# Kernel tuning notes

Hardware: AMD Instinct MI355X
Metric: run time of the kernel (lower is better)

## Reference

```python
import jax, jax.numpy as jnp
import numpy as np

D, HID, C = 300, 64, 21          # Dict_size, hidden_size, cell_size
B, H, W = 4, 144, 144

def gelu(x):
    return jax.nn.gelu(x, approximate=False)  # torch nn.GELU default (erf)

def c1x1(x, w, b):
    # 1x1 conv == pointwise matmul over channels: x [b,c,h,w], w [o,c], b [o]
    return jnp.einsum('bchw,oc->bohw', x, w) + b[None, :, None, None]

def gconv(x, w, b):
    return gelu(c1x1(x, w, b))


def setup_inputs() -> dict:
    key = jax.random.key(0)
    ks = iter(jax.random.split(key, 40))
    def Wm(o, i):
        return jax.random.normal(next(ks), (o, i), jnp.float32) * 0.05
    def bv(o):
        return jax.random.normal(next(ks), (o,), jnp.float32) * 0.01
    inp = {'y': jax.random.normal(next(ks), (B, C, H, W), jnp.float32)}
    # cell_size -> Dict_size encoders
    for nm in ['we1', 'we2', 'wfy1', 'wiy1', 'wfy2', 'wiy2']:
        inp[nm + '_w'] = Wm(D, C); inp[nm + '_b'] = bv(D)
    # Dict_size -> Dict_size recurrent convs
    for nm in ['wd1', 'wd2', 'wfx1', 'wix1', 'wfx2', 'wix2']:
        inp[nm + '_w'] = Wm(D, D); inp[nm + '_b'] = bv(D)
    # Line1 head: 3x3 valid conv D->2*HID, then 1x1 2*HID->2*HID, 1x1 2*HID->1
    inp['line_w1'] = jax.random.normal(next(ks), (2 * HID, D, 3, 3), jnp.float32) * 0.05
    inp['line_b1'] = bv(2 * HID)
    inp['line_w2'] = Wm(2 * HID, 2 * HID); inp['line_b2'] = bv(2 * HID)
    inp['line_w3'] = Wm(1, 2 * HID);       inp['line_b3'] = bv(1)
    return inp


def reference(y, we1_w, we1_b, we2_w, we2_b, wfy1_w, wfy1_b, wiy1_w, wiy1_b,
              wfy2_w, wfy2_b, wiy2_w, wiy2_b, wd1_w, wd1_b, wd2_w, wd2_b,
              wfx1_w, wfx1_b, wix1_w, wix1_b, wfx2_w, wfx2_b, wix2_w, wix2_b,
              line_w1, line_b1, line_w2, line_b2, line_w3, line_b3):
    ywe1 = gconv(y, we1_w, we1_b)
    ywe2 = gconv(y, we2_w, we2_b)
    ywfy1 = gconv(y, wfy1_w, wfy1_b)
    ywiy1 = gconv(y, wiy1_w, wiy1_b)
    ywfy2 = gconv(y, wfy2_w, wfy2_b)
    ywiy2 = gconv(y, wiy2_w, wiy2_b)

    def step2(x12, c12, xt1):  # first half-cell (the '2' gates)
        ctlide1 = ywe2 + xt1 - gconv(x12, wd2_w, wd2_b)
        ft1 = jax.nn.sigmoid(gconv(x12, wfx2_w, wfx2_b) + ywfy2)
        it1 = jax.nn.sigmoid(gconv(x12, wix2_w, wix2_b) + ywiy2)
        ct1 = c12 * ft1 + ctlide1 * it1
        return ct1, jax.nn.relu(ct1)

    xt1 = jnp.float32(0.0)
    c12 = jax.nn.sigmoid(ywiy1) * (-ywe1)
    x12 = jax.nn.relu(c12)

    for _ in range(3):
        ct1, xt1 = step2(x12, c12, xt1)
        c1tlide = ywe1 + xt1 - gconv(xt1, wd1_w, wd1_b)
        ft21 = jax.nn.sigmoid(gconv(xt1, wfx1_w, wfx1_b) + ywfy1)
        it21 = jax.nn.sigmoid(gconv(xt1, wix1_w, wix1_b) + ywiy1)
        ct2 = ct1 * ft21 + c1tlide * it21
        x12 = jax.nn.relu(ct2)
        c12 = ct2

    ct1, xt1 = step2(x12, c12, xt1)

    # Line1: 3x3 valid conv + GELU, 1x1 + GELU, 1x1
    h = jax.lax.conv_general_dilated(
        xt1, line_w1, window_strides=(1, 1), padding='VALID',
        dimension_numbers=('NCHW', 'OIHW', 'NCHW')) + line_b1[None, :, None, None]
    h = gelu(h)
    h = gelu(c1x1(h, line_w2, line_b2))
    return c1x1(h, line_w3, line_b3)
```

## Files before the change

### kernel.cpp

```cpp
#include <hip/hip_runtime.h>

typedef _Float16 f16;
typedef _Float16 f16x8 __attribute__((ext_vector_type(8)));
typedef _Float16 f16x4 __attribute__((ext_vector_type(4)));
typedef float    f32x4 __attribute__((ext_vector_type(4)));

#define NP      82944
#define NPIX_B  20736
#define KP      320
#define OC      128
#define NP2     80656
#define NOC     15
#define OCH     20
#define GN      192
#define GBUF    24576

__device__ __forceinline__ float geluf(float x) {
    return 0.5f * x * (1.0f + erff(x * 0.70710678118654752f));
}
__device__ __forceinline__ float sigm(float x) {
    return 1.0f / (1.0f + __expf(-x));
}
__device__ __forceinline__ f32x4 mfma16(f16x8 a, f16x8 b, f32x4 c) {
    return __builtin_amdgcn_mfma_f32_16x16x32_f16(a, b, c, 0, 0, 0);
}
__device__ __forceinline__ void gload_lds16(const void* g, void* l) {
    __builtin_amdgcn_global_load_lds(
        (const __attribute__((address_space(1))) void*)g,
        (__attribute__((address_space(3))) void*)l, 16, 0, 0);
}
__device__ __forceinline__ int xcd_swz(int bid, int nwg) {
    int q = nwg >> 3, r = nwg & 7;
    int xcd = bid & 7, idx = bid >> 3;
    return (xcd < r ? xcd * (q + 1) : r * (q + 1) + (xcd - r) * q) + idx;
}

__global__ __launch_bounds__(64) void pack_gate_w(
    const float* __restrict__ wd2, const float* __restrict__ wfx2, const float* __restrict__ wix2,
    const float* __restrict__ wd1, const float* __restrict__ wfx1, const float* __restrict__ wix1,
    const float* __restrict__ bd2, const float* __restrict__ bfx2, const float* __restrict__ bix2,
    const float* __restrict__ bd1, const float* __restrict__ bfx1, const float* __restrict__ bix1,
    f16* __restrict__ wpk2, f16* __restrict__ wpk1,
    float* __restrict__ bpk2, float* __restrict__ bpk1)
{
    int bid = blockIdx.x;
    int o = bid % KP;
    int g = (bid / KP) % 3;
    int s = bid / (KP * 3);
    const float* wsrc; const float* bsrc;
    if (s == 0) { wsrc = (g==0)?wd2:((g==1)?wfx2:wix2); bsrc = (g==0)?bd2:((g==1)?bfx2:bix2); }
    else        { wsrc = (g==0)?wd1:((g==1)?wfx1:wix1); bsrc = (g==0)?bd1:((g==1)?bfx1:bix1); }
    f16* wdst = (s==0 ? wpk2 : wpk1) + ((size_t)g*KP + o)*KP;
    int t = threadIdx.x;
#pragma unroll
    for (int i = 0; i < 5; ++i) {
        int k = i*64 + t;
        wdst[k] = (o < 300 && k < 300) ? (f16)wsrc[o*300 + k] : (f16)0.0f;
    }
    if (t == 0) {
        float* bd = (s==0 ? bpk2 : bpk1);
        bd[g*KP + o] = (o < 300) ? bsrc[o] : 0.0f;
    }
}

__global__ __launch_bounds__(64) void pack_line_w(
    const float* __restrict__ lw1, const float* __restrict__ lw2,
    f16* __restrict__ w1p, f16* __restrict__ w2p)
{
    int bid = blockIdx.x;
    int t = threadIdx.x;
    if (bid < 9*OC) {
        int t9 = bid / OC, oc = bid % OC;
        f16* dst = w1p + ((size_t)t9*OC + oc)*KP;
#pragma unroll
        for (int i = 0; i < 5; ++i) {
            int k = i*64 + t;
            dst[k] = (k < 300) ? (f16)lw1[(size_t)(oc*300 + k)*9 + t9] : (f16)0.0f;
        }
    } else {
        int oc = bid - 9*OC;
        f16* dst = w2p + (size_t)oc*OC;
#pragma unroll
        for (int i = 0; i < 2; ++i) {
            int k = i*64 + t;
            dst[k] = (f16)lw2[oc*OC + k];
        }
    }
}

__global__ __launch_bounds__(256) void encoder_kernel(
    const float* __restrict__ y,
    const float* __restrict__ w_e1, const float* __restrict__ b_e1,
    const float* __restrict__ w_e2, const float* __restrict__ b_e2,
    const float* __restrict__ w_f1, const float* __restrict__ b_f1,
    const float* __restrict__ w_i1, const float* __restrict__ b_i1,
    const float* __restrict__ w_f2, const float* __restrict__ b_f2,
    const float* __restrict__ w_i2, const float* __restrict__ b_i2,
    f16* __restrict__ enc, float* __restrict__ cbuf, f16* __restrict__ xa,
    int p_off, int chpx)
{
    int lid = xcd_swz(blockIdx.x, gridDim.x);
    int oc = lid % NOC;
    int pb = lid / NOC;
    int p  = pb * 256 + threadIdx.x;
    if (p >= chpx) return;
    int o0 = oc * OCH;
    int gp = p_off + p;
    int b = gp / NPIX_B, pin = gp % NPIX_B;
    const float* yb = y + (size_t)b*21*NPIX_B + pin;
    float yv[21];
#pragma unroll
    for (int c = 0; c < 21; ++c) yv[c] = yb[(size_t)c * NPIX_B];

    size_t rowbase = (size_t)p*KP + o0;
    size_t estr = (size_t)chpx*KP;

#define ENC_ONE(W, B, EIDX)                                            \
    {                                                                  \
        f16* dst = enc + (size_t)(EIDX)*estr + rowbase;                \
        _Pragma("unroll 1")                                            \
        for (int rq = 0; rq < 5; ++rq) {                               \
            f16x4 st;                                                  \
            _Pragma("unroll")                                          \
            for (int j = 0; j < 4; ++j) {                              \
                int r = rq*4 + j;                                      \
                const float* wr = (W) + (o0 + r)*21;                   \
                float acc = (B)[o0 + r];                               \
                _Pragma("unroll")                                      \
                for (int c = 0; c < 21; ++c) acc = fmaf(wr[c], yv[c], acc); \
                st[j] = (f16)geluf(acc);                               \
            }                                                          \
            *(f16x4*)(dst + rq*4) = st;                                \
        }                                                              \
    }

    ENC_ONE(w_e1, b_e1, 0)
    ENC_ONE(w_e2, b_e2, 1)
    ENC_ONE(w_f1, b_f1, 2)
    ENC_ONE(w_i1, b_i1, 3)
    ENC_ONE(w_f2, b_f2, 4)
    ENC_ONE(w_i2, b_i2, 5)
#undef ENC_ONE

#pragma unroll 1
    for (int rq = 0; rq < 5; ++rq) {
        f16x4 v0 = *(const f16x4*)(enc + (size_t)0*estr + rowbase + rq*4);
        f16x4 v3 = *(const f16x4*)(enc + (size_t)3*estr + rowbase + rq*4);
        f32x4 cv; f16x4 xv;
#pragma unroll
        for (int j = 0; j < 4; ++j) {
            float c12 = sigm((float)v3[j]) * (-(float)v0[j]);
            cv[j] = c12;
            xv[j] = (f16)fmaxf(c12, 0.0f);
        }
        *(f32x4*)(cbuf + rowbase + rq*4) = cv;
        *(f16x4*)(xa + rowbase + rq*4) = xv;
    }
}

__global__ __launch_bounds__(256) void gate_kernel(
    const f16* __restrict__ xin, const f16* __restrict__ wpk,
    const float* __restrict__ bpk,
    const f16* __restrict__ ey, const f16* __restrict__ fy,
    const f16* __restrict__ iy, const f16* __restrict__ ad,
    float* __restrict__ cio, f16* __restrict__ xout, int first, int chpx)
{
    __shared__ uint4 smem4[2*GBUF/16];
    char* smem = (char*)smem4;
    int tid = threadIdx.x;
    int l = tid & 63, w = tid >> 6;
    int lr = l & 15, lh = l >> 4;
    int lid = xcd_swz(blockIdx.x, gridDim.x);
    int mt = lid % 10, nt = lid / 10;
    int o0 = mt * 32;
    int p0 = nt * GN;

    const char* srcb[6];
#pragma unroll
    for (int j = 0; j < 6; ++j) {
        int c = j*256 + tid;
        if (c < 480) {
            int row = c / 5, slot = c % 5; if (slot > 3) slot = 0;
            int g = row >> 5, o = o0 + (row & 31);
            srcb[j] = (const char*)wpk + ((size_t)g*KP + o)*(KP*2) + slot*16;
        } else if (c < 1440) {
            int cb = c - 480;
            int row = cb / 5, slot = cb % 5; if (slot > 3) slot = 0;
            srcb[j] = (const char*)xin + (size_t)(p0 + row)*(KP*2) + slot*16;
        } else {
            srcb[j] = (const char*)xin;
        }
    }

#define GSTAGE(BUF, KS)                                                \
    {                                                                  \
        int kb = (KS)*64;                                              \
        _Pragma("unroll")                                              \
        for (int j = 0; j < 6; ++j)                                    \
            gload_lds16(srcb[j] + kb, &smem[(BUF)*GBUF + (j*256+tid)*16]); \
    }

    f32x4 acc[3][2][3] = {};
    GSTAGE(0, 0)

    int buf = 0;
#pragma unroll 1
    for (int ks = 0; ks < 10; ++ks) {
        if (ks < 9) {
            GSTAGE(buf^1, ks+1)
            asm volatile("s_waitcnt vmcnt(6)" ::: "memory");
        } else {
            asm volatile("s_waitcnt vmcnt(0)" ::: "memory");
        }
        __builtin_amdgcn_s_barrier();
        f16x8 bfr[3];
#pragma unroll
        for (int n = 0; n < 3; ++n)
            bfr[n] = *(const f16x8*)&smem[buf*GBUF + 7680 + (w*48 + n*16 + lr)*80 + lh*16];
#pragma unroll
        for (int g = 0; g < 3; ++g) {
#pragma unroll
            for (int m = 0; m < 2; ++m) {
                f16x8 a = *(const f16x8*)&smem[buf*GBUF + (g*32 + m*16 + lr)*80 + lh*16];
#pragma unroll
                for (int n = 0; n < 3; ++n)
                    acc[g][m][n] = mfma16(a, bfr[n], acc[g][m][n]);
            }
        }
        if (ks < 9) __builtin_amdgcn_s_barrier();
        buf ^= 1;
    }
#undef GSTAGE

#pragma unroll
    for (int m = 0; m < 2; ++m) {
        int o = o0 + m*16 + lh*4;
        if (o >= 300) continue;
        f32x4 bd = *(const f32x4*)(bpk + 0*KP + o);
        f32x4 bf = *(const f32x4*)(bpk + 1*KP + o);
        f32x4 bi = *(const f32x4*)(bpk + 2*KP + o);
#pragma unroll
        for (int n = 0; n < 3; ++n) {
            int p = p0 + w*48 + n*16 + lr;
            if (p >= chpx) continue;
            size_t base = (size_t)p*KP + o;
            f16x4 vey = *(const f16x4*)(ey + base);
            f16x4 vfy = *(const f16x4*)(fy + base);
            f16x4 viy = *(const f16x4*)(iy + base);
            f32x4 vci = *(const f32x4*)(cio + base);
            f16x4 vad = {};
            if (!first) vad = *(const f16x4*)(ad + base);
            f32x4 co; f16x4 xo;
#pragma unroll
            for (int r = 0; r < 4; ++r) {
                float gd = geluf(acc[0][m][n][r] + bd[r]);
                float gf = geluf(acc[1][m][n][r] + bf[r]);
                float gi = geluf(acc[2][m][n][r] + bi[r]);
                float addv = first ? 0.0f : (float)vad[r];
                float ctl = (float)vey[r] + addv - gd;
                float ft  = sigm(gf + (float)vfy[r]);
                float it  = sigm(gi + (float)viy[r]);
                float ct  = vci[r]*ft + ctl*it;
                co[r] = ct;
                xo[r] = (f16)fmaxf(ct, 0.0f);
            }
            *(f32x4*)(cio + base) = co;
            *(f16x4*)(xout + base) = xo;
        }
    }
}

__global__ __launch_bounds__(256) void conv3_kernel(
    const f16* __restrict__ xt, const f16* __restrict__ w1p,
    const float* __restrict__ b1, f16* __restrict__ h1)
{
    __shared__ uint4 smem4[750];
    char* smem = (char*)smem4;
    int tid = threadIdx.x;
    int l = tid & 63, w = tid >> 6;
    int lr = l & 15, lh = l >> 4;
    int lid = xcd_swz(blockIdx.x, gridDim.x);
    int xs = lid % 3;
    int by = lid / 3;
    int b = by / 142, yy = by % 142;
    int x0 = xs * 48;

    const char* sp[3];
    int dstb[3];
    bool act[3];
#pragma unroll
    for (int j = 0; j < 3; ++j) {
        int c = j*256 + tid;
        act[j] = (c < 600);
        int cc = act[j] ? c : 599;
        int row = cc >> 2, slot = cc & 3;
        int dy = row / 50, pxo = row % 50;
        int gx = x0 + pxo; if (gx > 143) gx = 143;
        size_t gp = (size_t)((b*144 + yy + dy)*144 + gx);
        sp[j] = (const char*)xt + gp*(KP*2) + slot*16;
        dstb[j] = row*80 + slot*16;
    }

    uint4 regs[3];
#pragma unroll
    for (int j = 0; j < 3; ++j) regs[j] = *(const uint4*)(sp[j]);

    f32x4 acc[2][3] = {};
#pragma unroll 1
    for (int ks = 0; ks < 10; ++ks) {
#pragma unroll
        for (int j = 0; j < 3; ++j)
            if (act[j]) *(uint4*)&smem[dstb[j]] = regs[j];
        __syncthreads();
        if (ks < 9) {
            int kb = (ks+1)*64;
#pragma unroll
            for (int j = 0; j < 3; ++j) regs[j] = *(const uint4*)(sp[j] + kb);
        }
        int k0 = ks*32;
#pragma unroll 3
        for (int t9 = 0; t9 < 9; ++t9) {
            int dy = t9 / 3, dx = t9 % 3;
            const f16* ap = w1p + ((size_t)(t9*OC + w*32 + lr))*KP + k0 + lh*8;
            f16x8 a0 = *(const f16x8*)ap;
            f16x8 a1 = *(const f16x8*)(ap + (size_t)16*KP);
#pragma unroll
            for (int n = 0; n < 3; ++n) {
                int row = dy*50 + dx + n*16 + lr;
                f16x8 bv = *(const f16x8*)&smem[row*80 + lh*16];
                acc[0][n] = mfma16(a0, bv, acc[0][n]);
                acc[1][n] = mfma16(a1, bv, acc[1][n]);
            }
        }
        __syncthreads();
    }

#pragma unroll
    for (int m = 0; m < 2; ++m) {
        int ocb = w*32 + m*16 + lh*4;
        f32x4 bb = *(const f32x4*)(b1 + ocb);
#pragma unroll
        for (int n = 0; n < 3; ++n) {
            int x = x0 + n*16 + lr;
            if (x < 142) {
                int pout = (b*142 + yy)*142 + x;
                f16x4 hv;
#pragma unroll
                for (int r = 0; r < 4; ++r) hv[r] = (f16)geluf(acc[m][n][r] + bb[r]);
                *(f16x4*)(h1 + (size_t)pout*OC + ocb) = hv;
            }
        }
    }
}

__global__ __launch_bounds__(256) void gemm128_kernel(
    const f16* __restrict__ hin, const f16* __restrict__ w2p,
    const float* __restrict__ b2, f16* __restrict__ hout)
{
    int tid = threadIdx.x;
    int l = tid & 63, w = tid >> 6;
    int lr = l & 15, lh = l >> 4;
    int bid = blockIdx.x;
    int mt = bid & 3, nt = bid >> 2;
    int p0 = nt * 128 + w * 32;
    if (p0 >= NP2) return;
    int o0 = mt * 32;

    f32x4 acc[2][2] = {};
    int pr0 = min(p0 + lr,      NP2 - 1);
    int pr1 = min(p0 + 16 + lr, NP2 - 1);
    const f16* bp0 = hin + (size_t)pr0*OC + lh*8;
    const f16* bp1 = hin + (size_t)pr1*OC + lh*8;
    const f16* ap  = w2p + (size_t)(o0 + lr)*OC + lh*8;
#pragma unroll
    for (int k0 = 0; k0 < OC; k0 += 32) {
        f16x8 b0  = *(const f16x8*)(bp0 + k0);
        f16x8 b1v = *(const f16x8*)(bp1 + k0);
#pragma unroll
        for (int m = 0; m < 2; ++m) {
            f16x8 a = *(const f16x8*)(ap + (size_t)m*16*OC + k0);
            acc[m][0] = mfma16(a, b0,  acc[m][0]);
            acc[m][1] = mfma16(a, b1v, acc[m][1]);
        }
    }
#pragma unroll
    for (int m = 0; m < 2; ++m) {
        int oc = o0 + m*16 + lh*4;
        f32x4 bb = *(const f32x4*)(b2 + oc);
#pragma unroll
        for (int n = 0; n < 2; ++n) {
            int p = p0 + n*16 + lr;
            if (p < NP2) {
                f16x4 hv;
#pragma unroll
                for (int r = 0; r < 4; ++r) hv[r] = (f16)geluf(acc[m][n][r] + bb[r]);
                *(f16x4*)(hout + (size_t)p*OC + oc) = hv;
            }
        }
    }
}

__global__ __launch_bounds__(256) void final_dot_kernel(
    const f16* __restrict__ h2, const float* __restrict__ w3,
    const float* __restrict__ b3, float* __restrict__ out)
{
    int p = blockIdx.x * 256 + threadIdx.x;
    if (p >= NP2) return;
    const f16x8* row = (const f16x8*)(h2 + (size_t)p * OC);
    float acc = 0.0f;
#pragma unroll
    for (int i = 0; i < 16; ++i) {
        f16x8 v = row[i];
#pragma unroll
        for (int j = 0; j < 8; ++j) acc = fmaf((float)v[j], w3[i*8 + j], acc);
    }
    out[p] = acc + b3[0];
}

extern "C" void kernel_launch(void* const* d_in, const int* in_sizes, int n_in,
                              void* d_out, int out_size, void* d_ws, size_t ws_size,
                              hipStream_t stream)
{
    const float* y      = (const float*)d_in[0];
    const float* we1_w  = (const float*)d_in[1];  const float* we1_b  = (const float*)d_in[2];
    const float* we2_w  = (const float*)d_in[3];  const float* we2_b  = (const float*)d_in[4];
    const float* wfy1_w = (const float*)d_in[5];  const float* wfy1_b = (const float*)d_in[6];
    const float* wiy1_w = (const float*)d_in[7];  const float* wiy1_b = (const float*)d_in[8];
    const float* wfy2_w = (const float*)d_in[9];  const float* wfy2_b = (const float*)d_in[10];
    const float* wiy2_w = (const float*)d_in[11]; const float* wiy2_b = (const float*)d_in[12];
    const float* wd1_w  = (const float*)d_in[13]; const float* wd1_b  = (const float*)d_in[14];
    const float* wd2_w  = (const float*)d_in[15]; const float* wd2_b  = (const float*)d_in[16];
    const float* wfx1_w = (const float*)d_in[17]; const float* wfx1_b = (const float*)d_in[18];
    const float* wix1_w = (const float*)d_in[19]; const float* wix1_b = (const float*)d_in[20];
    const float* wfx2_w = (const float*)d_in[21]; const float* wfx2_b = (const float*)d_in[22];
    const float* wix2_w = (const float*)d_in[23]; const float* wix2_b = (const float*)d_in[24];
    const float* line_w1 = (const float*)d_in[25]; const float* line_b1 = (const float*)d_in[26];
    const float* line_w2 = (const float*)d_in[27]; const float* line_b2 = (const float*)d_in[28];
    const float* line_w3 = (const float*)d_in[29]; const float* line_b3 = (const float*)d_in[30];
    float* out = (float*)d_out;

    auto padb = [](size_t b){ return (b + 255) & ~(size_t)255; };
    auto need = [&](int ch)->size_t {
        size_t chpx = (size_t)NP / ch;
        size_t s = 0;
        s += padb(6*chpx*KP*2);
        s += 2*padb(chpx*KP*2);
        s += padb(chpx*KP*4);
        s += padb((size_t)NP*KP*2);
        s += 2*padb((size_t)3*KP*KP*2);
        s += 2*padb((size_t)3*KP*4);
        s += padb((size_t)9*OC*KP*2);
        s += padb((size_t)OC*OC*2);
        return s;
    };
    const int CHN = (need(4) <= ws_size) ? 4 : 8;
    const int chpx = NP / CHN;

    char* base = (char*)d_ws;
    size_t off = 0;
    auto take = [&](size_t bytes) -> void* {
        void* r = base + off;
        off += (bytes + 255) & ~(size_t)255;
        return r;
    };
    char* chunk_base = base;
    f16*   enc  = (f16*)take((size_t)6 * chpx * KP * sizeof(f16));
    f16*   xa   = (f16*)take((size_t)chpx * KP * sizeof(f16));
    f16*   xb   = (f16*)take((size_t)chpx * KP * sizeof(f16));
    float* cbuf = (float*)take((size_t)chpx * KP * sizeof(float));
    f16* xt1full = (f16*)take((size_t)NP * KP * sizeof(f16));
    f16* wpk2 = (f16*)take((size_t)3 * KP * KP * sizeof(f16));
    f16* wpk1 = (f16*)take((size_t)3 * KP * KP * sizeof(f16));
    float* bpk2 = (float*)take((size_t)3 * KP * sizeof(float));
    float* bpk1 = (float*)take((size_t)3 * KP * sizeof(float));
    f16* w1p = (f16*)take((size_t)9 * OC * KP * sizeof(f16));
    f16* w2p = (f16*)take((size_t)OC * OC * sizeof(f16));
    f16* h1 = (f16*)chunk_base;
    f16* h2 = (f16*)(chunk_base + (size_t)NP2 * OC * sizeof(f16));
    if (off > ws_size) return;

    pack_gate_w<<<2*3*KP, 64, 0, stream>>>(wd2_w, wfx2_w, wix2_w, wd1_w, wfx1_w, wix1_w,
                                           wd2_b, wfx2_b, wix2_b, wd1_b, wfx1_b, wix1_b,
                                           wpk2, wpk1, bpk2, bpk1);
    pack_line_w<<<9*OC + OC, 64, 0, stream>>>(line_w1, line_w2, w1p, w2p);

    const int EGRID = ((chpx + 255) / 256) * NOC;
    const int GGRID = (chpx / GN) * 10;
    f16* e0 = enc + (size_t)0*chpx*KP;
    f16* e1 = enc + (size_t)1*chpx*KP;
    f16* e2 = enc + (size_t)2*chpx*KP;
    f16* e3 = enc + (size_t)3*chpx*KP;
    f16* e4 = enc + (size_t)4*chpx*KP;
    f16* e5 = enc + (size_t)5*chpx*KP;

    for (int c = 0; c < CHN; ++c) {
        int p_off = c * chpx;
        encoder_kernel<<<EGRID, 256, 0, stream>>>(y,
            we1_w, we1_b, we2_w, we2_b, wfy1_w, wfy1_b, wiy1_w, wiy1_b,
            wfy2_w, wfy2_b, wiy2_w, wiy2_b,
            enc, cbuf, xa, p_off, chpx);

        gate_kernel<<<GGRID, 256, 0, stream>>>(xa, wpk2, bpk2, e1, e4, e5, xb, cbuf, xb, 1, chpx);
        for (int it = 0; it < 3; ++it) {
            gate_kernel<<<GGRID, 256, 0, stream>>>(xb, wpk1, bpk1, e0, e2, e3, xb, cbuf, xa, 0, chpx);
            f16* xo = (it == 2) ? (xt1full + (size_t)p_off * KP) : xb;
            gate_kernel<<<GGRID, 256, 0, stream>>>(xa, wpk2, bpk2, e1, e4, e5, xb, cbuf, xo, 0, chpx);
        }
    }

    conv3_kernel<<<568*3, 256, 0, stream>>>(xt1full, w1p, line_b1, h1);
    gemm128_kernel<<<((NP2 + 127)/128) * 4, 256, 0, stream>>>(h1, w2p, line_b2, h2);
    final_dot_kernel<<<(NP2 + 255)/256, 256, 0, stream>>>(h2, line_w3, line_b3, out);
}
```

Baseline: 2.305 ms.

## Widen conv3 tiles, hoist gate epilogue loads, regroup encoder channels

The 3x3 conv kernel now computes 96 output pixels per block instead of 48. That doubles accumulator count and LDS use but reuses each weight fragment load across twice as many MFMAs, with fewer blocks. The gate kernel epilogue issues all elementwise operand loads before the GELU/sigmoid math and gains an occupancy hint of 3 blocks per CU, aiming to overlap memory latency. The encoder splits channels into 10 groups of 32 with clamped rows, in place of 15 groups of 20, so it does redundant work on the padded channels. Dropping the bounds checks ahead of the epilogue loads relies on the padded buffers staying in range.

```diff
diff --git a/kernel.cpp b/kernel.cpp
--- a/kernel.cpp
+++ b/kernel.cpp
@@ -10,8 +10,8 @@
 #define KP      320
 #define OC      128
 #define NP2     80656
-#define NOC     15
-#define OCH     20
+#define NOC     10
+#define OCH     32
 #define GN      192
 #define GBUF    24576
 
@@ -119,13 +119,13 @@
     {                                                                  \
         f16* dst = enc + (size_t)(EIDX)*estr + rowbase;                \
         _Pragma("unroll 1")                                            \
-        for (int rq = 0; rq < 5; ++rq) {                               \
+        for (int rq = 0; rq < OCH/4; ++rq) {                           \
             f16x4 st;                                                  \
             _Pragma("unroll")                                          \
             for (int j = 0; j < 4; ++j) {                              \
-                int r = rq*4 + j;                                      \
-                const float* wr = (W) + (o0 + r)*21;                   \
-                float acc = (B)[o0 + r];                               \
+                int r = o0 + rq*4 + j; if (r > 299) r = 299;           \
+                const float* wr = (W) + r*21;                          \
+                float acc = (B)[r];                                    \
                 _Pragma("unroll")                                      \
                 for (int c = 0; c < 21; ++c) acc = fmaf(wr[c], yv[c], acc); \
                 st[j] = (f16)geluf(acc);                               \
@@ -143,7 +143,7 @@
 #undef ENC_ONE
 
 #pragma unroll 1
-    for (int rq = 0; rq < 5; ++rq) {
+    for (int rq = 0; rq < OCH/4; ++rq) {
         f16x4 v0 = *(const f16x4*)(enc + (size_t)0*estr + rowbase + rq*4);
         f16x4 v3 = *(const f16x4*)(enc + (size_t)3*estr + rowbase + rq*4);
         f32x4 cv; f16x4 xv;
@@ -158,7 +158,7 @@
     }
 }
 
-__global__ __launch_bounds__(256) void gate_kernel(
+__global__ __launch_bounds__(256, 3) void gate_kernel(
     const f16* __restrict__ xin, const f16* __restrict__ wpk,
     const float* __restrict__ bpk,
     const f16* __restrict__ ey, const f16* __restrict__ fy,
@@ -235,37 +235,42 @@
 #pragma unroll
     for (int m = 0; m < 2; ++m) {
         int o = o0 + m*16 + lh*4;
-        if (o >= 300) continue;
         f32x4 bd = *(const f32x4*)(bpk + 0*KP + o);
         f32x4 bf = *(const f32x4*)(bpk + 1*KP + o);
         f32x4 bi = *(const f32x4*)(bpk + 2*KP + o);
+        size_t bas[3];
+        f16x4 vey[3], vfy[3], viy[3], vad[3];
+        f32x4 vci[3];
 #pragma unroll
         for (int n = 0; n < 3; ++n) {
             int p = p0 + w*48 + n*16 + lr;
-            if (p >= chpx) continue;
             size_t base = (size_t)p*KP + o;
-            f16x4 vey = *(const f16x4*)(ey + base);
-            f16x4 vfy = *(const f16x4*)(fy + base);
-            f16x4 viy = *(const f16x4*)(iy + base);
-            f32x4 vci = *(const f32x4*)(cio + base);
-            f16x4 vad = {};
-            if (!first) vad = *(const f16x4*)(ad + base);
+            bas[n] = base;
+            vey[n] = *(const f16x4*)(ey + base);
+            vfy[n] = *(const f16x4*)(fy + base);
+            viy[n] = *(const f16x4*)(iy + base);
+            vci[n] = *(const f32x4*)(cio + base);
+            if (!first) vad[n] = *(const f16x4*)(ad + base);
+            else        vad[n] = (f16x4){};
+        }
+        if (o >= 300) continue;
+#pragma unroll
+        for (int n = 0; n < 3; ++n) {
             f32x4 co; f16x4 xo;
 #pragma unroll
             for (int r = 0; r < 4; ++r) {
                 float gd = geluf(acc[0][m][n][r] + bd[r]);
                 float gf = geluf(acc[1][m][n][r] + bf[r]);
                 float gi = geluf(acc[2][m][n][r] + bi[r]);
-                float addv = first ? 0.0f : (float)vad[r];
-                float ctl = (float)vey[r] + addv - gd;
-                float ft  = sigm(gf + (float)vfy[r]);
-                float it  = sigm(gi + (float)viy[r]);
-                float ct  = vci[r]*ft + ctl*it;
+                float ctl = (float)vey[n][r] + (float)vad[n][r] - gd;
+                float ft  = sigm(gf + (float)vfy[n][r]);
+                float it  = sigm(gi + (float)viy[n][r]);
+                float ct  = vci[n][r]*ft + ctl*it;
                 co[r] = ct;
                 xo[r] = (f16)fmaxf(ct, 0.0f);
             }
-            *(f32x4*)(cio + base) = co;
-            *(f16x4*)(xout + base) = xo;
+            *(f32x4*)(cio + bas[n]) = co;
+            *(f16x4*)(xout + bas[n]) = xo;
         }
     }
 }
@@ -274,48 +279,48 @@
     const f16* __restrict__ xt, const f16* __restrict__ w1p,
     const float* __restrict__ b1, f16* __restrict__ h1)
 {
-    __shared__ uint4 smem4[750];
+    __shared__ uint4 smem4[1470];
     char* smem = (char*)smem4;
     int tid = threadIdx.x;
     int l = tid & 63, w = tid >> 6;
     int lr = l & 15, lh = l >> 4;
     int lid = xcd_swz(blockIdx.x, gridDim.x);
-    int xs = lid % 3;
-    int by = lid / 3;
+    int xs = lid & 1;
+    int by = lid >> 1;
     int b = by / 142, yy = by % 142;
-    int x0 = xs * 48;
-
-    const char* sp[3];
-    int dstb[3];
-    bool act[3];
-#pragma unroll
-    for (int j = 0; j < 3; ++j) {
+    int x0 = xs * 96;
+
+    const char* sp[5];
+    int dstb[5];
+    bool act[5];
+#pragma unroll
+    for (int j = 0; j < 5; ++j) {
         int c = j*256 + tid;
-        act[j] = (c < 600);
-        int cc = act[j] ? c : 599;
+        act[j] = (c < 1176);
+        int cc = act[j] ? c : 1175;
         int row = cc >> 2, slot = cc & 3;
-        int dy = row / 50, pxo = row % 50;
+        int dy = row / 98, pxo = row % 98;
         int gx = x0 + pxo; if (gx > 143) gx = 143;
         size_t gp = (size_t)((b*144 + yy + dy)*144 + gx);
         sp[j] = (const char*)xt + gp*(KP*2) + slot*16;
         dstb[j] = row*80 + slot*16;
     }
 
-    uint4 regs[3];
-#pragma unroll
-    for (int j = 0; j < 3; ++j) regs[j] = *(const uint4*)(sp[j]);
-
-    f32x4 acc[2][3] = {};
+    uint4 regs[5];
+#pragma unroll
+    for (int j = 0; j < 5; ++j) regs[j] = *(const uint4*)(sp[j]);
+
+    f32x4 acc[2][6] = {};
 #pragma unroll 1
     for (int ks = 0; ks < 10; ++ks) {
 #pragma unroll
-        for (int j = 0; j < 3; ++j)
+        for (int j = 0; j < 5; ++j)
             if (act[j]) *(uint4*)&smem[dstb[j]] = regs[j];
         __syncthreads();
         if (ks < 9) {
             int kb = (ks+1)*64;
 #pragma unroll
-            for (int j = 0; j < 3; ++j) regs[j] = *(const uint4*)(sp[j] + kb);
+            for (int j = 0; j < 5; ++j) regs[j] = *(const uint4*)(sp[j] + kb);
         }
         int k0 = ks*32;
 #pragma unroll 3
@@ -325,8 +330,8 @@
             f16x8 a0 = *(const f16x8*)ap;
             f16x8 a1 = *(const f16x8*)(ap + (size_t)16*KP);
 #pragma unroll
-            for (int n = 0; n < 3; ++n) {
-                int row = dy*50 + dx + n*16 + lr;
+            for (int n = 0; n < 6; ++n) {
+                int row = dy*98 + dx + n*16 + lr;
                 f16x8 bv = *(const f16x8*)&smem[row*80 + lh*16];
                 acc[0][n] = mfma16(a0, bv, acc[0][n]);
                 acc[1][n] = mfma16(a1, bv, acc[1][n]);
@@ -340,7 +345,7 @@
         int ocb = w*32 + m*16 + lh*4;
         f32x4 bb = *(const f32x4*)(b1 + ocb);
 #pragma unroll
-        for (int n = 0; n < 3; ++n) {
+        for (int n = 0; n < 6; ++n) {
             int x = x0 + n*16 + lr;
             if (x < 142) {
                 int pout = (b*142 + yy)*142 + x;
@@ -508,7 +513,7 @@
         }
     }
 
-    conv3_kernel<<<568*3, 256, 0, stream>>>(xt1full, w1p, line_b1, h1);
+    conv3_kernel<<<568*2, 256, 0, stream>>>(xt1full, w1p, line_b1, h1);
     gemm128_kernel<<<((NP2 + 127)/128) * 4, 256, 0, stream>>>(h1, w2p, line_b2, h2);
     final_dot_kernel<<<(NP2 + 255)/256, 256, 0, stream>>>(h2, line_w3, line_b3, out);
 }
```

Result: slower. 2.522 ms (+9.4%).
